# Optimization experiments

Hardware: AMD Instinct MI355X
Metric: run time of the kernel (lower is better)

## Reference

```python
import jax, jax.numpy as jnp
import numpy as np

TEMP = 0.3
K_ANCHORS = 512
SK_ITERS = 4  # max_iter=4 in the original; tol early-exit omitted (fixed small iter count)
EPS = 1e-12   # F.normalize clamp_min eps


def setup_inputs() -> dict:
    key = jax.random.key(0)
    k1, k2 = jax.random.split(key)
    x = jax.random.normal(k1, (16, 256, 64, 64), dtype=jnp.float32)
    some_idx = jax.random.randint(k2, (K_ANCHORS,), 0, 64 * 64, dtype=jnp.int32)
    return {"x": x, "some_idx": some_idx}


def sinkhorn_knopp(A):
    # A: [M, k], strictly positive. Normalize by total mass, then alternate
    # L1 column / row normalization (p=1 normalize on positive entries == sum-divide).
    A = A / A.sum()
    def body(A, _):
        A = A / jnp.clip(A.sum(axis=0, keepdims=True), EPS)  # columns
        A = A / jnp.clip(A.sum(axis=1, keepdims=True), EPS)  # rows
        return A, None
    A, _ = jax.lax.scan(body, A, None, length=SK_ITERS)
    return A


def reference(x, some_idx):
    N, C, H, W = x.shape
    k = some_idx.shape[0]
    # L2-normalize over channel dim (F.normalize dim=1)
    l2_x = x / jnp.clip(jnp.linalg.norm(x, axis=1, keepdims=True), EPS)
    # gather k random spatial anchors -> [N, C, k]
    some_x = jnp.take(l2_x.reshape(N, C, H * W), some_idx, axis=-1)
    # cosine scores [N, k, H, W]
    scores = jnp.einsum('nchw,nck->nkhw', l2_x, some_x)
    # flatten to [N*H*W, k], exponentiate, Sinkhorn-Knopp
    A = jnp.exp(scores.transpose(0, 2, 3, 1).reshape(-1, k) / TEMP)
    A = sinkhorn_knopp(A)
    Kmat = A.reshape(N, H, W, k).transpose(0, 3, 1, 2)  # [N, k, H, W]
    # reconstruct from anchors
    return jnp.einsum('nkhw,nck->nchw', Kmat, some_x)
```

## Files before the change

### kernel.cpp

```cpp
#include <hip/hip_runtime.h>
#include <hip/hip_bf16.h>
#include <hip/hip_fp16.h>

#define N_B 16
#define C_DIM 256
#define HW 4096
#define M_TOT (N_B*HW)
#define K_A 512
#define TEMP_INV (1.0f/0.3f)
#define EPS_SK 1e-12f

typedef _Float16 f16x8 __attribute__((ext_vector_type(8)));
typedef _Float16 f16x4 __attribute__((ext_vector_type(4)));
typedef float f32x4 __attribute__((ext_vector_type(4)));

#define GLOBAL_AS __attribute__((address_space(1)))
#define LDS_AS __attribute__((address_space(3)))
__device__ __forceinline__ void gload_lds16(const void* g, void* l){
    __builtin_amdgcn_global_load_lds((GLOBAL_AS const void*)g, (LDS_AS void*)l, 16, 0, 0);
}

__global__ __launch_bounds__(256) void k_normtrans(const float* __restrict__ x,
                                                   _Float16* __restrict__ Lt,
                                                   float* __restrict__ u,
                                                   float* __restrict__ v,
                                                   unsigned* bcnt, unsigned* bgen){
    __shared__ float tl[32][257];
    __shared__ float red[8][32];
    __shared__ float invs[32];
    int n   = blockIdx.x >> 7;
    int hw0 = (blockIdx.x & 127) * 32;
    if (threadIdx.x < 32) u[blockIdx.x*32 + threadIdx.x] = 1.0f;
    if (blockIdx.x < 2)   v[blockIdx.x*256 + threadIdx.x] = 1.0f;
    if (blockIdx.x == 0 && threadIdx.x == 0){
        __hip_atomic_store(bcnt, 0u, __ATOMIC_RELAXED, __HIP_MEMORY_SCOPE_AGENT);
        __hip_atomic_store(bgen, 0u, __ATOMIC_RELAXED, __HIP_MEMORY_SCOPE_AGENT);
    }
    int tx4 = threadIdx.x & 7;
    int cy  = threadIdx.x >> 3;
    const float* px = x + ((size_t)(n*C_DIM + cy))*HW + hw0 + tx4*4;
    #pragma unroll
    for (int r = 0; r < 8; ++r){
        float4 xv = *(const float4*)(px + (size_t)(r*32)*HW);
        int c = cy + r*32;
        tl[tx4*4+0][c] = xv.x;
        tl[tx4*4+1][c] = xv.y;
        tl[tx4*4+2][c] = xv.z;
        tl[tx4*4+3][c] = xv.w;
    }
    __syncthreads();
    int tx = threadIdx.x & 31, ty = threadIdx.x >> 5;
    float ss = 0.f;
    #pragma unroll
    for (int cc = 0; cc < 32; ++cc){
        float tv = tl[tx][cc*8 + ty];
        ss += tv*tv;
    }
    red[ty][tx] = ss;
    __syncthreads();
    if (ty == 0){
        float s = red[0][tx]+red[1][tx]+red[2][tx]+red[3][tx]
                + red[4][tx]+red[5][tx]+red[6][tx]+red[7][tx];
        invs[tx] = 1.0f / fmaxf(sqrtf(s), 1e-12f);
    }
    __syncthreads();
    #pragma unroll
    for (int r = 0; r < 4; ++r){
        int hwl = ty + r*8;
        float inv = invs[hwl];
        f16x8 h;
        #pragma unroll
        for (int e = 0; e < 8; ++e) h[e] = (_Float16)(tl[hwl][tx*8 + e] * inv);
        *(f16x8*)&Lt[((size_t)(n*HW + hw0 + hwl))*C_DIM + tx*8] = h;
    }
}

__global__ __launch_bounds__(256) void k_gather(const _Float16* __restrict__ Lt,
                                                const int* __restrict__ sidx,
                                                _Float16* __restrict__ sxT){
    int n  = blockIdx.y;
    int jj = blockIdx.x*8 + (threadIdx.x >> 5);
    int c8 = (threadIdx.x & 31) * 8;
    int p  = sidx[jj];
    *(f16x8*)&sxT[((size_t)(n*K_A + jj))*C_DIM + c8] =
        *(const f16x8*)&Lt[((size_t)(n*HW + p))*C_DIM + c8];
}

__global__ __launch_bounds__(256) void k_gemm1(const _Float16* __restrict__ Lt,
                                               const _Float16* __restrict__ sxT,
                                               _Float16* __restrict__ A0,
                                               float* __restrict__ part){
    __shared__ _Float16 As[3*128*32];
    __shared__ _Float16 Bs[3*128*32];
    __shared__ float colred[4][128];
    const int swz = (blockIdx.x & 7)*256 + (blockIdx.x >> 3);
    const int jb = swz & 3, mb = (swz >> 2) & 31, nb = swz >> 7;
    const int mbase = mb * 128;
    const int jbase = jb * 128;
    const int t = threadIdx.x;
    const int lane = t & 63, w = t >> 6;
    const int wm = (w >> 1)*64, wn = (w & 1)*64;
    const int l15 = lane & 15, lq = lane >> 4;

    f32x4 acc[4][4] = {};
    const _Float16* pa = Lt  + ((size_t)(nb*HW  + mbase))*C_DIM;
    const _Float16* pb = sxT + ((size_t)(nb*K_A + jbase))*C_DIM;

    const int r0 = t >> 2, ch = t & 3;
    const int r1 = r0 + 64;
    const int cs0 = (ch ^ ((r0 >> 1) & 3)) << 3;
    const int cs1 = (ch ^ ((r1 >> 1) & 3)) << 3;

#define STAGE1(buf, kt) { int k0 = (kt)*32; \
    gload_lds16(pa + (size_t)r0*C_DIM + k0 + cs0, &As[(buf)*4096 + t*8]); \
    gload_lds16(pa + (size_t)r1*C_DIM + k0 + cs1, &As[(buf)*4096 + (256+t)*8]); \
    gload_lds16(pb + (size_t)r0*C_DIM + k0 + cs0, &Bs[(buf)*4096 + t*8]); \
    gload_lds16(pb + (size_t)r1*C_DIM + k0 + cs1, &Bs[(buf)*4096 + (256+t)*8]); }

    STAGE1(0, 0); STAGE1(1, 1); STAGE1(2, 2);
    #pragma unroll
    for (int kt = 0; kt < 8; ++kt){
        if (kt < 6)      asm volatile("s_waitcnt vmcnt(8)" ::: "memory");
        else if (kt < 7) asm volatile("s_waitcnt vmcnt(4)" ::: "memory");
        else             asm volatile("s_waitcnt vmcnt(0)" ::: "memory");
        __builtin_amdgcn_s_barrier();
        __builtin_amdgcn_sched_barrier(0);
        const int cur = kt % 3;
        f16x8 af[4], bf[4];
        #pragma unroll
        for (int mi = 0; mi < 4; ++mi){
            int r = wm + mi*16 + l15;
            af[mi] = *(const f16x8*)&As[cur*4096 + r*32 + ((lq ^ ((r>>1)&3)) << 3)];
        }
        #pragma unroll
        for (int ni = 0; ni < 4; ++ni){
            int r = wn + ni*16 + l15;
            bf[ni] = *(const f16x8*)&Bs[cur*4096 + r*32 + ((lq ^ ((r>>1)&3)) << 3)];
        }
        #pragma unroll
        for (int mi = 0; mi < 4; ++mi)
            #pragma unroll
            for (int ni = 0; ni < 4; ++ni)
                acc[mi][ni] = __builtin_amdgcn_mfma_f32_16x16x32_f16(af[mi], bf[ni], acc[mi][ni], 0, 0, 0);
        __builtin_amdgcn_s_barrier();
        __builtin_amdgcn_sched_barrier(0);
        if (kt < 5) STAGE1((kt+3)%3, kt+3);
    }
    float csum[4] = {0.f, 0.f, 0.f, 0.f};
    #pragma unroll
    for (int mi = 0; mi < 4; ++mi)
        #pragma unroll
        for (int ni = 0; ni < 4; ++ni)
            #pragma unroll
            for (int r = 0; r < 4; ++r){
                int hw = mbase + wm + mi*16 + lq*4 + r;
                int j  = jbase + wn + ni*16 + l15;
                float e = __expf(acc[mi][ni][r] * TEMP_INV);
                A0[((size_t)(nb*HW + hw))*K_A + j] = (_Float16)e;
                csum[ni] += e;
            }
    #pragma unroll
    for (int ni = 0; ni < 4; ++ni){
        float cv = csum[ni];
        cv += __shfl_xor(cv, 16);
        cv += __shfl_xor(cv, 32);
        if (lane < 16) colred[w][wn + ni*16 + l15] = cv;
    }
    __syncthreads();
    if (t < 128){
        int jj = t;
        float s = (jj < 64) ? (colred[0][jj] + colred[2][jj])
                            : (colred[1][jj] + colred[3][jj]);
        part[((size_t)(nb*32 + mb))*K_A + jbase + jj] = s;
    }
}

__global__ __launch_bounds__(64) void k_colfinish(const float* __restrict__ part,
                                                  float* __restrict__ v, int nchunks){
    int j = blockIdx.x;
    int lane = threadIdx.x;
    float s = 0.f;
    for (int r = lane; r < nchunks; r += 64) s += part[(size_t)r*K_A + j];
    #pragma unroll
    for (int off = 32; off; off >>= 1) s += __shfl_xor(s, off);
    if (lane == 0){
        float vo = v[j];
        v[j] = 128.0f * vo / fmaxf(vo * s, EPS_SK);
    }
}

__global__ __launch_bounds__(256) void k_fused(const _Float16* __restrict__ A0,
                                               const float* __restrict__ v,
                                               float* __restrict__ u,
                                               float* __restrict__ part){
    __shared__ float red[4][512];
    int b = blockIdx.x;
    int tg = threadIdx.x >> 6, lane = threadIdx.x & 63;
    float vr[8];
    const float* pv = v + (lane << 3);
    #pragma unroll
    for (int e = 0; e < 8; ++e) vr[e] = pv[e];
    float acc[8] = {};
    for (int it = 0; it < 16; ++it){
        int i = (b << 6) + (it << 2) + tg;
        f16x8 a = *(const f16x8*)&A0[(size_t)i*K_A + (lane << 3)];
        float r = 0.f;
        #pragma unroll
        for (int e = 0; e < 8; ++e) r += (float)a[e] * vr[e];
        #pragma unroll
        for (int off = 32; off; off >>= 1) r += __shfl_xor(r, off);
        float uo = u[i];
        float un = uo / fmaxf(uo * r, EPS_SK);
        if (lane == 0) u[i] = un;
        #pragma unroll
        for (int e = 0; e < 8; ++e) acc[e] += (float)a[e] * un;
    }
    #pragma unroll
    for (int e = 0; e < 8; ++e) red[tg][(lane<<3)+e] = acc[e];
    __syncthreads();
    if (tg == 0){
        #pragma unroll
        for (int e = 0; e < 8; ++e){
            int j = (lane<<3)+e;
            part[((size_t)b)*K_A + j] = red[0][j]+red[1][j]+red[2][j]+red[3][j];
        }
    }
}

__device__ __forceinline__ void gbar(unsigned* cnt, unsigned* gen){
    __threadfence();
    __syncthreads();
    if (threadIdx.x == 0){
        unsigned g = __hip_atomic_load(gen, __ATOMIC_RELAXED, __HIP_MEMORY_SCOPE_AGENT);
        unsigned a = __hip_atomic_fetch_add(cnt, 1u, __ATOMIC_ACQ_REL, __HIP_MEMORY_SCOPE_AGENT);
        if (a == 511u){
            __hip_atomic_store(cnt, 0u, __ATOMIC_RELAXED, __HIP_MEMORY_SCOPE_AGENT);
            __hip_atomic_store(gen, g + 1u, __ATOMIC_RELEASE, __HIP_MEMORY_SCOPE_AGENT);
        } else {
            while (__hip_atomic_load(gen, __ATOMIC_ACQUIRE, __HIP_MEMORY_SCOPE_AGENT) == g)
                __builtin_amdgcn_s_sleep(8);
        }
    }
    __syncthreads();
    __threadfence();
}

__device__ __forceinline__ void colfin(const float* part, float* v, int b, int t){
    if (t < 64){
        float s = 0.f;
        #pragma unroll
        for (int g = 0; g < 8; ++g)
            s += __hip_atomic_load(&part[(size_t)(t + g*64)*K_A + b],
                                   __ATOMIC_RELAXED, __HIP_MEMORY_SCOPE_AGENT);
        #pragma unroll
        for (int off = 32; off; off >>= 1) s += __shfl_xor(s, off);
        if (t == 0){
            float vo = __hip_atomic_load(&v[b], __ATOMIC_RELAXED, __HIP_MEMORY_SCOPE_AGENT);
            __hip_atomic_store(&v[b], 128.0f * vo / fmaxf(vo * s, EPS_SK),
                               __ATOMIC_RELAXED, __HIP_MEMORY_SCOPE_AGENT);
        }
    }
}

__global__ __launch_bounds__(512, 4) void k_sink(const _Float16* __restrict__ A0,
                                                 float* v, float* u, float* part,
                                                 unsigned* bcnt, unsigned* bgen){
    __shared__ float red[8][512];
    const int b = blockIdx.x, t = threadIdx.x;
    const int tg = t >> 6, lane = t & 63;
    const int i0 = (b << 7) + tg;
    f16x8 a[16];
    float ur[16];
    #pragma unroll
    for (int it = 0; it < 16; ++it){
        a[it] = *(const f16x8*)&A0[(size_t)(i0 + it*8)*K_A + (lane<<3)];
        ur[it] = 1.0f;
    }
    colfin(part, v, b, t);
    gbar(bcnt, bgen);
    float vr[8];
    #pragma unroll
    for (int e = 0; e < 8; ++e)
        vr[e] = __hip_atomic_load(&v[(lane<<3)+e], __ATOMIC_RELAXED, __HIP_MEMORY_SCOPE_AGENT);
    for (int t3 = 0; t3 < 3; ++t3){
        if (t3){
            gbar(bcnt, bgen);
            #pragma unroll
            for (int e = 0; e < 8; ++e)
                vr[e] = __hip_atomic_load(&v[(lane<<3)+e], __ATOMIC_RELAXED, __HIP_MEMORY_SCOPE_AGENT);
        }
        #pragma unroll
        for (int it = 0; it < 16; ++it){
            float r = 0.f;
            #pragma unroll
            for (int e = 0; e < 8; ++e) r += (float)a[it][e] * vr[e];
            #pragma unroll
            for (int off = 32; off; off >>= 1) r += __shfl_xor(r, off);
            ur[it] = ur[it] / fmaxf(ur[it] * r, EPS_SK);
        }
        float acc[8] = {0.f,0.f,0.f,0.f,0.f,0.f,0.f,0.f};
        #pragma unroll
        for (int it = 0; it < 16; ++it)
            #pragma unroll
            for (int e = 0; e < 8; ++e) acc[e] += (float)a[it][e] * ur[it];
        #pragma unroll
        for (int e = 0; e < 8; ++e) red[tg][(lane<<3)+e] = acc[e];
        __syncthreads();
        {
            float s = red[0][t]+red[1][t]+red[2][t]+red[3][t]
                    + red[4][t]+red[5][t]+red[6][t]+red[7][t];
            __hip_atomic_store(&part[(size_t)b*K_A + t], s,
                               __ATOMIC_RELAXED, __HIP_MEMORY_SCOPE_AGENT);
        }
        gbar(bcnt, bgen);
        colfin(part, v, b, t);
    }
    if (lane == 0){
        #pragma unroll
        for (int it = 0; it < 16; ++it) u[i0 + it*8] = ur[it];
    }
}

__global__ __launch_bounds__(256) void k_sxvT(const _Float16* __restrict__ sxT,
                                              const float* __restrict__ v,
                                              _Float16* __restrict__ SXv){
    __shared__ float tl[64][65];
    int n  = blockIdx.z;
    int j0 = blockIdx.x * 64;
    int c0 = blockIdx.y * 64;
    int tx = threadIdx.x & 63, ty = threadIdx.x >> 6;
    #pragma unroll
    for (int r = 0; r < 16; ++r){
        int jl = ty + r*4;
        tl[jl][tx] = (float)sxT[((size_t)(n*K_A + j0 + jl))*C_DIM + c0 + tx] * v[j0 + jl];
    }
    __syncthreads();
    #pragma unroll
    for (int r = 0; r < 16; ++r){
        int cl = ty + r*4;
        SXv[((size_t)(n*C_DIM + c0 + cl))*K_A + j0 + tx] = (_Float16)tl[tx][cl];
    }
}

__global__ __launch_bounds__(256) void k_gemm2(const _Float16* __restrict__ SXv,
                                               const _Float16* __restrict__ A0,
                                               const float* __restrict__ v,
                                               const float* __restrict__ u,
                                               float* __restrict__ out){
    __shared__ _Float16 As[3*128*32];
    __shared__ _Float16 Bs[3*128*32];
    __shared__ _Float16 vsh[512];
    const int swz = (blockIdx.x & 7)*128 + (blockIdx.x >> 3);
    const int mb = swz & 1, nbi = (swz >> 1) & 31, nb = swz >> 6;
    const int mbase = mb * 128;
    const int nbase = nbi * 128;
    const int t = threadIdx.x;
    const int lane = t & 63, w = t >> 6;
    const int wm = (w >> 1)*64, wn = (w & 1)*64;
    const int l15 = lane & 15, lq = lane >> 4;

    vsh[t]       = (_Float16)v[t];
    vsh[t + 256] = (_Float16)v[t + 256];

    f32x4 acc[4][4] = {};
    f32x4 racc[4] = {};
    const _Float16* pa = SXv + ((size_t)(nb*C_DIM + mbase))*K_A;
    const _Float16* pb = A0  + ((size_t)(nb*HW   + nbase))*K_A;

    const int r0 = t >> 2, ch = t & 3;
    const int r1 = r0 + 64;
    const int cs0 = (ch ^ ((r0 >> 1) & 3)) << 3;
    const int cs1 = (ch ^ ((r1 >> 1) & 3)) << 3;

#define STAGE2(buf, kt) { int k0 = (kt)*32; \
    gload_lds16(pa + (size_t)r0*K_A + k0 + cs0, &As[(buf)*4096 + t*8]); \
    gload_lds16(pa + (size_t)r1*K_A + k0 + cs1, &As[(buf)*4096 + (256+t)*8]); \
    gload_lds16(pb + (size_t)r0*K_A + k0 + cs0, &Bs[(buf)*4096 + t*8]); \
    gload_lds16(pb + (size_t)r1*K_A + k0 + cs1, &Bs[(buf)*4096 + (256+t)*8]); }

    STAGE2(0, 0); STAGE2(1, 1); STAGE2(2, 2);
    #pragma unroll
    for (int kt = 0; kt < 16; ++kt){
        if (kt < 14)      asm volatile("s_waitcnt vmcnt(8)" ::: "memory");
        else if (kt < 15) asm volatile("s_waitcnt vmcnt(4)" ::: "memory");
        else              asm volatile("s_waitcnt vmcnt(0)" ::: "memory");
        __builtin_amdgcn_s_barrier();
        __builtin_amdgcn_sched_barrier(0);
        const int cur = kt % 3;
        f16x8 af[4], bf[4], vf;
        vf = *(const f16x8*)&vsh[kt*32 + lq*8];
        #pragma unroll
        for (int mi = 0; mi < 4; ++mi){
            int r = wm + mi*16 + l15;
            af[mi] = *(const f16x8*)&As[cur*4096 + r*32 + ((lq ^ ((r>>1)&3)) << 3)];
        }
        #pragma unroll
        for (int ni = 0; ni < 4; ++ni){
            int r = wn + ni*16 + l15;
            bf[ni] = *(const f16x8*)&Bs[cur*4096 + r*32 + ((lq ^ ((r>>1)&3)) << 3)];
        }
        #pragma unroll
        for (int mi = 0; mi < 4; ++mi)
            #pragma unroll
            for (int ni = 0; ni < 4; ++ni)
                acc[mi][ni] = __builtin_amdgcn_mfma_f32_16x16x32_f16(af[mi], bf[ni], acc[mi][ni], 0, 0, 0);
        #pragma unroll
        for (int ni = 0; ni < 4; ++ni)
            racc[ni] = __builtin_amdgcn_mfma_f32_16x16x32_f16(vf, bf[ni], racc[ni], 0, 0, 0);
        __builtin_amdgcn_s_barrier();
        __builtin_amdgcn_sched_barrier(0);
        if (kt < 13) STAGE2((kt+3)%3, kt+3);
    }
    float un[4];
    #pragma unroll
    for (int ni = 0; ni < 4; ++ni){
        float rv = racc[ni][0];
        float uo = u[nb*HW + nbase + wn + ni*16 + l15];
        un[ni] = uo / fmaxf(uo * rv, EPS_SK);
    }
    #pragma unroll
    for (int mi = 0; mi < 4; ++mi)
        #pragma unroll
        for (int ni = 0; ni < 4; ++ni)
            #pragma unroll
            for (int r = 0; r < 4; ++r){
                int c  = mbase + wm + mi*16 + lq*4 + r;
                int hw = nbase + wn + ni*16 + l15;
                out[((size_t)(nb*C_DIM + c))*HW + hw] = acc[mi][ni][r] * un[ni];
            }
}

extern "C" void kernel_launch(void* const* d_in, const int* in_sizes, int n_in,
                              void* d_out, int out_size, void* d_ws, size_t ws_size,
                              hipStream_t stream){
    const float* x  = (const float*)d_in[0];
    const int* sidx = (const int*)d_in[1];
    float* out = (float*)d_out;

    char* ws = (char*)d_ws;
    _Float16* Lt  = (_Float16*)ws;  ws += (size_t)N_B*HW*C_DIM*2;
    _Float16* A0  = (_Float16*)ws;  ws += (size_t)M_TOT*K_A*2;
    _Float16* sxT = (_Float16*)ws;  ws += (size_t)N_B*K_A*C_DIM*2;
    _Float16* SXv = (_Float16*)ws;  ws += (size_t)N_B*C_DIM*K_A*2;
    float*    u   = (float*)ws;     ws += (size_t)M_TOT*4;
    float*    v   = (float*)ws;     ws += (size_t)K_A*4;
    float*    part= (float*)ws;     ws += (size_t)1024*K_A*4;
    unsigned* bcnt= (unsigned*)ws;  ws += 256;
    unsigned* bgen= (unsigned*)ws;  ws += 256;

    k_normtrans<<<2048, 256, 0, stream>>>(x, Lt, u, v, bcnt, bgen);
    k_gather   <<<dim3(64,16), 256, 0, stream>>>(Lt, sidx, sxT);
    k_gemm1    <<<2048, 256, 0, stream>>>(Lt, sxT, A0, part);

    int occ = 0;
    hipError_t oe = hipOccupancyMaxActiveBlocksPerMultiprocessor(&occ, k_sink, 512, 0);
    bool coop = (oe == hipSuccess) && (occ >= 2);
    if (coop){
        void* kargs[] = { (void*)&A0, (void*)&v, (void*)&u, (void*)&part,
                          (void*)&bcnt, (void*)&bgen };
        coop = (hipLaunchCooperativeKernel((void*)k_sink, dim3(512), dim3(512),
                                           kargs, 0, stream) == hipSuccess);
    }
    if (!coop){
        k_colfinish<<<512, 64, 0, stream>>>(part, v, 512);
        for (int it = 0; it < 3; ++it){
            k_fused    <<<1024, 256, 0, stream>>>(A0, v, u, part);
            k_colfinish<<<512, 64, 0, stream>>>(part, v, 1024);
        }
    }

    k_sxvT <<<dim3(8,4,16), 256, 0, stream>>>(sxT, v, SXv);
    k_gemm2<<<1024, 256, 0, stream>>>(SXv, A0, v, u, out);
}
```

Before: 158.1 us.

## Use 256 persistent 1024-thread blocks for Sinkhorn and drop cooperative launch

The persistent Sinkhorn kernel now runs with 256 blocks of 1024 threads instead of 512 blocks of 512, so each block owns 256 rows. This halves the number of grid-barrier participants and partial column sums. Column finalisation now gives each block two columns and loops over a variable number of partial-sum chunks. The cooperative launch is replaced by a plain launch gated on register and attribute checks, and the barrier spin gets a timeout. The plain launch gives up the guarantee that all blocks are co-resident, which the kernel needs to avoid deadlock, and a timed-out barrier would silently give wrong results.

```diff
diff --git a/kernel.cpp b/kernel.cpp
--- a/kernel.cpp
+++ b/kernel.cpp
@@ -227,64 +227,68 @@
     }
 }
 
-__device__ __forceinline__ void gbar(unsigned* cnt, unsigned* gen){
+__device__ __forceinline__ void gbar256(unsigned* cnt, unsigned* gen){
     __threadfence();
     __syncthreads();
     if (threadIdx.x == 0){
         unsigned g = __hip_atomic_load(gen, __ATOMIC_RELAXED, __HIP_MEMORY_SCOPE_AGENT);
         unsigned a = __hip_atomic_fetch_add(cnt, 1u, __ATOMIC_ACQ_REL, __HIP_MEMORY_SCOPE_AGENT);
-        if (a == 511u){
+        if (a == 255u){
             __hip_atomic_store(cnt, 0u, __ATOMIC_RELAXED, __HIP_MEMORY_SCOPE_AGENT);
             __hip_atomic_store(gen, g + 1u, __ATOMIC_RELEASE, __HIP_MEMORY_SCOPE_AGENT);
         } else {
-            while (__hip_atomic_load(gen, __ATOMIC_ACQUIRE, __HIP_MEMORY_SCOPE_AGENT) == g)
+            unsigned spin = 0;
+            while (__hip_atomic_load(gen, __ATOMIC_ACQUIRE, __HIP_MEMORY_SCOPE_AGENT) == g){
                 __builtin_amdgcn_s_sleep(8);
+                if (++spin > (1u<<22)) break;
+            }
         }
     }
     __syncthreads();
     __threadfence();
 }
 
-__device__ __forceinline__ void colfin(const float* part, float* v, int b, int t){
-    if (t < 64){
+__device__ __forceinline__ void colfin2(const float* part, float* v, int b, int t, int nchunks){
+    int tg = t >> 6, lane = t & 63;
+    if (tg < 2){
+        int j = b*2 + tg;
         float s = 0.f;
-        #pragma unroll
-        for (int g = 0; g < 8; ++g)
-            s += __hip_atomic_load(&part[(size_t)(t + g*64)*K_A + b],
+        for (int r = lane; r < nchunks; r += 64)
+            s += __hip_atomic_load(&part[(size_t)r*K_A + j],
                                    __ATOMIC_RELAXED, __HIP_MEMORY_SCOPE_AGENT);
         #pragma unroll
         for (int off = 32; off; off >>= 1) s += __shfl_xor(s, off);
-        if (t == 0){
-            float vo = __hip_atomic_load(&v[b], __ATOMIC_RELAXED, __HIP_MEMORY_SCOPE_AGENT);
-            __hip_atomic_store(&v[b], 128.0f * vo / fmaxf(vo * s, EPS_SK),
+        if (lane == 0){
+            float vo = __hip_atomic_load(&v[j], __ATOMIC_RELAXED, __HIP_MEMORY_SCOPE_AGENT);
+            __hip_atomic_store(&v[j], 128.0f * vo / fmaxf(vo * s, EPS_SK),
                                __ATOMIC_RELAXED, __HIP_MEMORY_SCOPE_AGENT);
         }
     }
 }
 
-__global__ __launch_bounds__(512, 4) void k_sink(const _Float16* __restrict__ A0,
-                                                 float* v, float* u, float* part,
-                                                 unsigned* bcnt, unsigned* bgen){
-    __shared__ float red[8][512];
+__global__ __launch_bounds__(1024, 4) void k_sink(const _Float16* __restrict__ A0,
+                                                  float* v, float* u, float* part,
+                                                  unsigned* bcnt, unsigned* bgen){
+    __shared__ float red[16][512];
     const int b = blockIdx.x, t = threadIdx.x;
     const int tg = t >> 6, lane = t & 63;
-    const int i0 = (b << 7) + tg;
+    const int i0 = (b << 8) + tg;
     f16x8 a[16];
     float ur[16];
     #pragma unroll
     for (int it = 0; it < 16; ++it){
-        a[it] = *(const f16x8*)&A0[(size_t)(i0 + it*8)*K_A + (lane<<3)];
+        a[it] = *(const f16x8*)&A0[(size_t)(i0 + it*16)*K_A + (lane<<3)];
         ur[it] = 1.0f;
     }
-    colfin(part, v, b, t);
-    gbar(bcnt, bgen);
+    colfin2(part, v, b, t, 512);
+    gbar256(bcnt, bgen);
     float vr[8];
     #pragma unroll
     for (int e = 0; e < 8; ++e)
         vr[e] = __hip_atomic_load(&v[(lane<<3)+e], __ATOMIC_RELAXED, __HIP_MEMORY_SCOPE_AGENT);
     for (int t3 = 0; t3 < 3; ++t3){
         if (t3){
-            gbar(bcnt, bgen);
+            gbar256(bcnt, bgen);
             #pragma unroll
             for (int e = 0; e < 8; ++e)
                 vr[e] = __hip_atomic_load(&v[(lane<<3)+e], __ATOMIC_RELAXED, __HIP_MEMORY_SCOPE_AGENT);
@@ -306,18 +310,19 @@
         #pragma unroll
         for (int e = 0; e < 8; ++e) red[tg][(lane<<3)+e] = acc[e];
         __syncthreads();
-        {
-            float s = red[0][t]+red[1][t]+red[2][t]+red[3][t]
-                    + red[4][t]+red[5][t]+red[6][t]+red[7][t];
+        if (t < K_A){
+            float s = 0.f;
+            #pragma unroll
+            for (int g = 0; g < 16; ++g) s += red[g][t];
             __hip_atomic_store(&part[(size_t)b*K_A + t], s,
                                __ATOMIC_RELAXED, __HIP_MEMORY_SCOPE_AGENT);
         }
-        gbar(bcnt, bgen);
-        colfin(part, v, b, t);
+        gbar256(bcnt, bgen);
+        colfin2(part, v, b, t, 256);
     }
     if (lane == 0){
         #pragma unroll
-        for (int it = 0; it < 16; ++it) u[i0 + it*8] = ur[it];
+        for (int it = 0; it < 16; ++it) u[i0 + it*16] = ur[it];
     }
 }
 
@@ -452,16 +457,13 @@
     k_gather   <<<dim3(64,16), 256, 0, stream>>>(Lt, sidx, sxT);
     k_gemm1    <<<2048, 256, 0, stream>>>(Lt, sxT, A0, part);
 
-    int occ = 0;
-    hipError_t oe = hipOccupancyMaxActiveBlocksPerMultiprocessor(&occ, k_sink, 512, 0);
-    bool coop = (oe == hipSuccess) && (occ >= 2);
-    if (coop){
-        void* kargs[] = { (void*)&A0, (void*)&v, (void*)&u, (void*)&part,
-                          (void*)&bcnt, (void*)&bgen };
-        coop = (hipLaunchCooperativeKernel((void*)k_sink, dim3(512), dim3(512),
-                                           kargs, 0, stream) == hipSuccess);
-    }
-    if (!coop){
+    hipFuncAttributes attr{};
+    bool ok = (hipFuncGetAttributes(&attr, (const void*)k_sink) == hipSuccess)
+              && attr.localSizeBytes == 0 && attr.numRegs <= 128
+              && attr.maxThreadsPerBlock >= 1024;
+    if (ok){
+        k_sink<<<256, 1024, 0, stream>>>(A0, v, u, part, bcnt, bgen);
+    } else {
         k_colfinish<<<512, 64, 0, stream>>>(part, v, 512);
         for (int it = 0; it < 3; ++it){
             k_fused    <<<1024, 256, 0, stream>>>(A0, v, u, part);
```

New measurement: 156.8 us. No clear change (-0.8%).
